# Optimization experiments

Hardware: AMD Instinct MI355X
Metric: run time of the kernel (lower is better)

## Reference

```python
import jax, jax.numpy as jnp
import numpy as np

TEMPERATURE = 0.07
EPS = 1e-12  # matches torch F.normalize default eps


def setup_inputs() -> dict:
    key = jax.random.key(0)
    k1, k2 = jax.random.split(key)
    features1 = jax.random.normal(k1, (16384, 512), dtype=jnp.float32)
    features2 = jax.random.normal(k2, (16384, 512), dtype=jnp.float32)
    return {"features1": features1, "features2": features2}


def _l2_normalize(x):
    # torch F.normalize: x / max(||x||, eps)
    norm = jnp.sqrt(jnp.sum(x * x, axis=1, keepdims=True))
    return x / jnp.maximum(norm, EPS)


def reference(features1, features2):
    f1 = _l2_normalize(features1)
    f2 = _l2_normalize(features2)
    # [N, N] similarity logits
    logits = jnp.einsum('nd,md->nm', f1, f2) / TEMPERATURE
    n = logits.shape[0]
    # cross-entropy with labels = arange(n): mean over rows of (logsumexp - diag logit)
    log_probs = jax.nn.log_softmax(logits, axis=1)
    diag = jnp.diagonal(log_probs)
    loss = -jnp.mean(diag)
    return loss
```

## Files before the change

kernel.cpp:

```cpp
#include <hip/hip_runtime.h>
#include <stdint.h>

#define NROWS 16384
#define KDIM  512
#define BM 128
#define BN 256
#define CT 2
#define NCHUNK 32
#define NPH 16
#define SLOT 24576
#define INV_T 14.285714285714286f
#define LOG2E 1.4426950408889634f
#define LN2   0.6931471805599453f

typedef __bf16 bf16x8 __attribute__((ext_vector_type(8)));
typedef float  f32x16 __attribute__((ext_vector_type(16)));
typedef unsigned short u16x8 __attribute__((ext_vector_type(8)));

__device__ __forceinline__ void gload_lds16(const void* gptr, void* lptr) {
    uint32_t loff = (uint32_t)(uintptr_t)lptr;
    loff = __builtin_amdgcn_readfirstlane(loff);
    __builtin_amdgcn_global_load_lds(
        (const uint32_t __attribute__((address_space(1)))*)(uintptr_t)gptr,
        (uint32_t __attribute__((address_space(3)))*)(uintptr_t)loff,
        16, 0, 0);
}


__global__ void k_norm(const float* __restrict__ X, char* __restrict__ Y, float scale) {
    const int row  = blockIdx.x * 4 + (threadIdx.x >> 6);
    const int lane = threadIdx.x & 63;
    const float* xr = X + (size_t)row * KDIM + lane * 8;
    float4 a = *(const float4*)xr;
    float4 b = *(const float4*)(xr + 4);
    float ss = a.x*a.x + a.y*a.y + a.z*a.z + a.w*a.w
             + b.x*b.x + b.y*b.y + b.z*b.z + b.w*b.w;
    #pragma unroll
    for (int off = 1; off < 64; off <<= 1) ss += __shfl_xor(ss, off);
    const float s = scale / fmaxf(sqrtf(ss), 1e-12f);
    __bf16 o[8];
    o[0] = (__bf16)(a.x * s); o[1] = (__bf16)(a.y * s);
    o[2] = (__bf16)(a.z * s); o[3] = (__bf16)(a.w * s);
    o[4] = (__bf16)(b.x * s); o[5] = (__bf16)(b.y * s);
    o[6] = (__bf16)(b.z * s); o[7] = (__bf16)(b.w * s);
    const int kh = lane >> 2, q = lane & 3;
    const size_t gr = ((size_t)(kh * 512 + (row >> 5)) * 2 + (q >> 1)) * 64
                    + ((q & 1) << 5) + (row & 31);
    *(u16x8*)(Y + gr * 16) = *(const u16x8*)o;
}

__global__ __launch_bounds__(256, 1) void k_gemm(const char* __restrict__ A,
                                                 const char* __restrict__ B,
                                                 float* __restrict__ S_part) {
    __shared__ __align__(16) char L[3 * SLOT];
    __shared__ float rowsum[2][BM];
    char* Lc = (char*)L;

    const int tid  = threadIdx.x;
    const int lane = tid & 63;
    const int w    = tid >> 6;
    const int wr   = w >> 1, wc = w & 1;
    const int bid  = blockIdx.x;
    const int xcd  = bid & 7;
    const int idx  = bid >> 3;
    const int st   = idx >> 5;
    const int wsub = idx & 31;
    const int sg   = xcd * 16 + st;
    const int bg   = sg & 15, cg = sg >> 4;
    const int brow  = (bg * 8 + (wsub >> 2)) * BM;
    const int chunk = cg * 4 + (wsub & 3);
    const int rbA0 = brow >> 5;

#define STGA(KH_, S_) do {                                                    \
        const char* g_ = A + ((size_t)((KH_) * 512 + rbA0) * 2048) + tid * 16;\
        char* l_ = Lc + (S_) * SLOT + tid * 16;                               \
        gload_lds16(g_,        l_);                                           \
        gload_lds16(g_ + 4096, l_ + 4096);                                    \
    } while (0)

#define STGB(KH_, S_) do {                                                    \
        const char* g_ = B + ((size_t)((KH_) * 512 + rbB0) * 2048) + tid * 16;\
        char* l_ = Lc + (S_) * SLOT + 8192 + tid * 16;                        \
        gload_lds16(g_,         l_);                                          \
        gload_lds16(g_ +  4096, l_ +  4096);                                  \
        gload_lds16(g_ +  8192, l_ +  8192);                                  \
        gload_lds16(g_ + 12288, l_ + 12288);                                  \
    } while (0)

#define RDS(HH_) do {                                                         \
        const char* sl_ = Lc + ((HH_) % 3) * SLOT;                            \
        _Pragma("unroll") for (int m_ = 0; m_ < 2; ++m_)                      \
        _Pragma("unroll") for (int ks_ = 0; ks_ < 2; ++ks_)                   \
            af[m_][ks_] = *(const bf16x8*)(sl_ + ((wr * 2 + m_) << 11)        \
                                           + (ks_ << 10) + (lane << 4));      \
        _Pragma("unroll") for (int n_ = 0; n_ < 4; ++n_)                      \
        _Pragma("unroll") for (int ks_ = 0; ks_ < 2; ++ks_)                   \
            bf[n_][ks_] = *(const bf16x8*)(sl_ + 8192                         \
                  + ((wc * 4 + n_) << 11) + (ks_ << 10) + (lane << 4));       \
    } while (0)

#define MM() do {                                                             \
        __builtin_amdgcn_s_setprio(1);                                        \
        _Pragma("unroll") for (int m_ = 0; m_ < 2; ++m_)                      \
        _Pragma("unroll") for (int n_ = 0; n_ < 4; ++n_)                      \
        _Pragma("unroll") for (int ks_ = 0; ks_ < 2; ++ks_)                   \
            acc[m_][n_] = __builtin_amdgcn_mfma_f32_32x32x16_bf16(            \
                af[m_][ks_], bf[n_][ks_], acc[m_][n_], 0, 0, 0);              \
        __builtin_amdgcn_s_setprio(0);                                        \
    } while (0)

    float rowacc = 0.f;
    #pragma unroll 1
    for (int ct = 0; ct < CT; ++ct) {
        const int rbB0 = chunk * 16 + ct * 8;
        f32x16 acc[2][4] = {};
        bf16x8 af[2][2], bf[4][2];

        STGA(0, 0); STGB(0, 0);
        STGA(1, 1); STGB(1, 1);
        asm volatile("s_waitcnt vmcnt(6)" ::: "memory");
        __builtin_amdgcn_s_barrier();

        #pragma unroll
        for (int h = 0; h < NPH; ++h) {
            RDS(h);
            if (h < NPH - 2) { STGA(h + 2, (h + 2) % 3); STGB(h + 2, (h + 2) % 3); }
            MM();
            if (h < NPH - 2)       asm volatile("s_waitcnt vmcnt(6)" ::: "memory");
            else if (h == NPH - 2) asm volatile("s_waitcnt vmcnt(0)" ::: "memory");
            __builtin_amdgcn_s_barrier();
        }

        #pragma unroll
        for (int m = 0; m < 2; ++m) {
            float rs[16];
            #pragma unroll
            for (int r = 0; r < 16; ++r)
                rs[r] = __builtin_amdgcn_exp2f(acc[m][0][r])
                      + __builtin_amdgcn_exp2f(acc[m][1][r])
                      + __builtin_amdgcn_exp2f(acc[m][2][r])
                      + __builtin_amdgcn_exp2f(acc[m][3][r]);
            #pragma unroll
            for (int off = 16; off >= 1; off >>= 1)
                #pragma unroll
                for (int r = 0; r < 16; ++r)
                    rs[r] += __shfl_xor(rs[r], off);
            if ((lane & 31) == 0) {
                const int rb = wr * 64 + m * 32 + (lane >> 5) * 4;
                #pragma unroll
                for (int r = 0; r < 16; ++r)
                    rowsum[wc][rb + (r & 3) + 8 * (r >> 2)] = rs[r];
            }
        }
        __syncthreads();
        if (tid < BM) rowacc += rowsum[0][tid] + rowsum[1][tid];
        __syncthreads();
    }
#undef STGA
#undef STGB
#undef RDS
#undef MM
    if (tid < BM) S_part[(size_t)chunk * NROWS + brow + tid] = rowacc;
}

__global__ void k_diag(const char* __restrict__ A, const char* __restrict__ B,
                       float* __restrict__ diag) {
    const int row  = blockIdx.x * 4 + (threadIdx.x >> 6);
    const int lane = threadIdx.x & 63;
    const int kh = lane >> 2, q = lane & 3;
    const size_t gr = ((size_t)(kh * 512 + (row >> 5)) * 2 + (q >> 1)) * 64
                    + ((q & 1) << 5) + (row & 31);
    const bf16x8 va = *(const bf16x8*)(A + gr * 16);
    const bf16x8 vb = *(const bf16x8*)(B + gr * 16);
    float d = 0.f;
    #pragma unroll
    for (int i = 0; i < 8; ++i) d += (float)va[i] * (float)vb[i];
    #pragma unroll
    for (int off2 = 1; off2 < 64; off2 <<= 1) d += __shfl_xor(d, off2);
    if (lane == 0) diag[row] = d;
}

__global__ void k_loss(const float* __restrict__ S_part, const float* __restrict__ diag,
                       float* __restrict__ partial) {
    const int g = blockIdx.x * 256 + threadIdx.x;
    float S = 0.f;
    #pragma unroll
    for (int c = 0; c < NCHUNK; ++c) S += S_part[(size_t)c * NROWS + g];
    float v = logf(S) - diag[g] * LN2;
    __shared__ float wsum[4];
    #pragma unroll
    for (int off = 1; off < 64; off <<= 1) v += __shfl_xor(v, off);
    if ((threadIdx.x & 63) == 0) wsum[threadIdx.x >> 6] = v;
    __syncthreads();
    if (threadIdx.x == 0) partial[blockIdx.x] = wsum[0] + wsum[1] + wsum[2] + wsum[3];
}

__global__ void k_final(const float* __restrict__ partial, float* __restrict__ out) {
    float v = partial[threadIdx.x];
    #pragma unroll
    for (int off = 1; off < 64; off <<= 1) v += __shfl_xor(v, off);
    if (threadIdx.x == 0) out[0] = v * (1.0f / (float)NROWS);
}

extern "C" void kernel_launch(void* const* d_in, const int* in_sizes, int n_in,
                              void* d_out, int out_size, void* d_ws, size_t ws_size,
                              hipStream_t stream) {
    const float* f1 = (const float*)d_in[0];
    const float* f2 = (const float*)d_in[1];
    float* out = (float*)d_out;

    char* ws = (char*)d_ws;
    char*  f1p   = ws;
    char*  f2p   = ws + (16u << 20);
    float* S_part = (float*)(ws + (32u << 20));
    float* diag   = (float*)(ws + (34u << 20));
    float* part   = (float*)(ws + (34u << 20) + (1u << 16));

    k_norm<<<dim3(NROWS / 4), dim3(256), 0, stream>>>(f1, f1p, INV_T * LOG2E);
    k_norm<<<dim3(NROWS / 4), dim3(256), 0, stream>>>(f2, f2p, 1.0f);
    k_gemm<<<dim3((NROWS / BM) * NCHUNK), dim3(256), 0, stream>>>(f1p, f2p, S_part);
    k_diag<<<dim3(NROWS / 4), dim3(256), 0, stream>>>(f1p, f2p, diag);
    k_loss<<<dim3(NROWS / 256), dim3(256), 0, stream>>>(S_part, diag, part);
    k_final<<<dim3(1), dim3(64), 0, stream>>>(part, out);
}
```

Before: 341.7 us.

## Restructure GEMM: register-resident A from global, half-K B staging in LDS

The logsumexp GEMM now uses 256-row blocks where each wave loads its A fragments straight from global memory into a rotating register pipeline. B is staged in LDS in two 64 KB half-K buffers that are double-buffered across four column sub-chunks, which cuts per-phase barriers and lets row sums accumulate in registers instead of going through shared memory. The diagonal kernel now computes the fp32 cosine directly from the raw inputs, so the bf16 diagonal no longer matches the bf16 GEMM logits. This trades fewer LDS round-trips and barriers for higher register pressure and uncached global A loads inside the MFMA loop.

```diff
diff --git a/kernel.cpp b/kernel.cpp
--- a/kernel.cpp
+++ b/kernel.cpp
@@ -3,15 +3,10 @@
 
 #define NROWS 16384
 #define KDIM  512
-#define BM 128
-#define BN 256
-#define CT 2
+#define BM 256
 #define NCHUNK 32
-#define NPH 16
-#define SLOT 24576
 #define INV_T 14.285714285714286f
 #define LOG2E 1.4426950408889634f
-#define LN2   0.6931471805599453f
 
 typedef __bf16 bf16x8 __attribute__((ext_vector_type(8)));
 typedef float  f32x16 __attribute__((ext_vector_type(16)));
@@ -52,84 +47,77 @@
 __global__ __launch_bounds__(256, 1) void k_gemm(const char* __restrict__ A,
                                                  const char* __restrict__ B,
                                                  float* __restrict__ S_part) {
-    __shared__ __align__(16) char L[3 * SLOT];
-    __shared__ float rowsum[2][BM];
+    __shared__ __align__(16) char L[2 * 65536];
     char* Lc = (char*)L;
 
     const int tid  = threadIdx.x;
     const int lane = tid & 63;
     const int w    = tid >> 6;
-    const int wr   = w >> 1, wc = w & 1;
     const int bid  = blockIdx.x;
     const int xcd  = bid & 7;
     const int idx  = bid >> 3;
     const int st   = idx >> 5;
     const int wsub = idx & 31;
-    const int sg   = xcd * 16 + st;
-    const int bg   = sg & 15, cg = sg >> 4;
+    const int sg   = xcd * 8 + st;
+    const int bg   = sg & 7, cg = sg >> 3;
     const int brow  = (bg * 8 + (wsub >> 2)) * BM;
     const int chunk = cg * 4 + (wsub & 3);
     const int rbA0 = brow >> 5;
 
-#define STGA(KH_, S_) do {                                                    \
-        const char* g_ = A + ((size_t)((KH_) * 512 + rbA0) * 2048) + tid * 16;\
-        char* l_ = Lc + (S_) * SLOT + tid * 16;                               \
-        gload_lds16(g_,        l_);                                           \
-        gload_lds16(g_ + 4096, l_ + 4096);                                    \
-    } while (0)
-
-#define STGB(KH_, S_) do {                                                    \
-        const char* g_ = B + ((size_t)((KH_) * 512 + rbB0) * 2048) + tid * 16;\
-        char* l_ = Lc + (S_) * SLOT + 8192 + tid * 16;                        \
-        gload_lds16(g_,         l_);                                          \
-        gload_lds16(g_ +  4096, l_ +  4096);                                  \
-        gload_lds16(g_ +  8192, l_ +  8192);                                  \
-        gload_lds16(g_ + 12288, l_ + 12288);                                  \
-    } while (0)
-
-#define RDS(HH_) do {                                                         \
-        const char* sl_ = Lc + ((HH_) % 3) * SLOT;                            \
+#define STGH(C_, KH0_, BUFOFF_) do {                                          \
+        const int rbB_ = chunk * 16 + (C_) * 4;                               \
+        _Pragma("unroll") for (int kk_ = 0; kk_ < 8; ++kk_) {                 \
+            const char* g_ = B + ((size_t)(((KH0_) + kk_) * 512 + rbB_) * 2048) + tid * 16; \
+            char* l_ = Lc + (BUFOFF_) + kk_ * 8192 + tid * 16;                \
+            gload_lds16(g_, l_);                                              \
+            gload_lds16(g_ + 4096, l_ + 4096);                                \
+        }                                                                     \
+    } while (0)
+
+#define LOADA(KH0_, T_, S_) do {                                              \
         _Pragma("unroll") for (int m_ = 0; m_ < 2; ++m_)                      \
-        _Pragma("unroll") for (int ks_ = 0; ks_ < 2; ++ks_)                   \
-            af[m_][ks_] = *(const bf16x8*)(sl_ + ((wr * 2 + m_) << 11)        \
-                                           + (ks_ << 10) + (lane << 4));      \
+            aF[S_][m_] = *(const bf16x8*)(A                                   \
+                + ((size_t)((((KH0_) + ((T_) >> 1)) * 512 + rbA0 + w * 2 + m_) * 2 \
+                            + ((T_) & 1)) << 10) + (lane << 4));              \
+    } while (0)
+
+#define READB(T_, BUFOFF_, S_) do {                                           \
         _Pragma("unroll") for (int n_ = 0; n_ < 4; ++n_)                      \
-        _Pragma("unroll") for (int ks_ = 0; ks_ < 2; ++ks_)                   \
-            bf[n_][ks_] = *(const bf16x8*)(sl_ + 8192                         \
-                  + ((wc * 4 + n_) << 11) + (ks_ << 10) + (lane << 4));       \
-    } while (0)
-
-#define MM() do {                                                             \
-        __builtin_amdgcn_s_setprio(1);                                        \
-        _Pragma("unroll") for (int m_ = 0; m_ < 2; ++m_)                      \
-        _Pragma("unroll") for (int n_ = 0; n_ < 4; ++n_)                      \
-        _Pragma("unroll") for (int ks_ = 0; ks_ < 2; ++ks_)                   \
-            acc[m_][n_] = __builtin_amdgcn_mfma_f32_32x32x16_bf16(            \
-                af[m_][ks_], bf[n_][ks_], acc[m_][n_], 0, 0, 0);              \
-        __builtin_amdgcn_s_setprio(0);                                        \
-    } while (0)
-
-    float rowacc = 0.f;
+            bF[S_][n_] = *(const bf16x8*)(Lc + (BUFOFF_)                      \
+                + (((T_) >> 1) * 8192) + (n_ * 2048)                          \
+                + (((T_) & 1) << 10) + (lane << 4));                          \
+    } while (0)
+
+#define HALF(KH0_, BUFOFF_, STG_STMT_) do {                                   \
+        LOADA(KH0_, 0, 0); LOADA(KH0_, 1, 1); LOADA(KH0_, 2, 2);              \
+        LOADA(KH0_, 3, 3); LOADA(KH0_, 4, 4); LOADA(KH0_, 5, 5);              \
+        STG_STMT_;                                                            \
+        READB(0, BUFOFF_, 0);                                                 \
+        _Pragma("unroll") for (int tt_ = 0; tt_ < 16; ++tt_) {                \
+            if (tt_ < 15) READB(tt_ + 1, BUFOFF_, (tt_ + 1) & 1);             \
+            if (tt_ < 10) LOADA(KH0_, tt_ + 6, (tt_ + 6) % 6);                \
+            _Pragma("unroll") for (int m_ = 0; m_ < 2; ++m_)                  \
+            _Pragma("unroll") for (int n_ = 0; n_ < 4; ++n_)                  \
+                acc[m_][n_] = __builtin_amdgcn_mfma_f32_32x32x16_bf16(        \
+                    aF[tt_ % 6][m_], bF[tt_ & 1][n_], acc[m_][n_], 0, 0, 0);  \
+        }                                                                     \
+    } while (0)
+
+    bf16x8 aF[6][2], bF[2][4];
+    float rowacc[2][16] = {};
+
+    STGH(0, 0, 0);
+    asm volatile("s_waitcnt vmcnt(0)" ::: "memory");
+    __builtin_amdgcn_s_barrier();
+
     #pragma unroll 1
-    for (int ct = 0; ct < CT; ++ct) {
-        const int rbB0 = chunk * 16 + ct * 8;
+    for (int c = 0; c < 4; ++c) {
         f32x16 acc[2][4] = {};
-        bf16x8 af[2][2], bf[4][2];
-
-        STGA(0, 0); STGB(0, 0);
-        STGA(1, 1); STGB(1, 1);
-        asm volatile("s_waitcnt vmcnt(6)" ::: "memory");
+        HALF(0, 0, STGH(c, 8, 65536));
+        asm volatile("s_waitcnt vmcnt(0)" ::: "memory");
         __builtin_amdgcn_s_barrier();
-
-        #pragma unroll
-        for (int h = 0; h < NPH; ++h) {
-            RDS(h);
-            if (h < NPH - 2) { STGA(h + 2, (h + 2) % 3); STGB(h + 2, (h + 2) % 3); }
-            MM();
-            if (h < NPH - 2)       asm volatile("s_waitcnt vmcnt(6)" ::: "memory");
-            else if (h == NPH - 2) asm volatile("s_waitcnt vmcnt(0)" ::: "memory");
-            __builtin_amdgcn_s_barrier();
-        }
+        if (c < 3) { HALF(8, 65536, STGH(c + 1, 0, 0)); }
+        else       { HALF(8, 65536, ((void)0)); }
 
         #pragma unroll
         for (int m = 0; m < 2; ++m) {
@@ -145,39 +133,50 @@
                 #pragma unroll
                 for (int r = 0; r < 16; ++r)
                     rs[r] += __shfl_xor(rs[r], off);
-            if ((lane & 31) == 0) {
-                const int rb = wr * 64 + m * 32 + (lane >> 5) * 4;
-                #pragma unroll
-                for (int r = 0; r < 16; ++r)
-                    rowsum[wc][rb + (r & 3) + 8 * (r >> 2)] = rs[r];
-            }
+            #pragma unroll
+            for (int r = 0; r < 16; ++r) rowacc[m][r] += rs[r];
         }
-        __syncthreads();
-        if (tid < BM) rowacc += rowsum[0][tid] + rowsum[1][tid];
-        __syncthreads();
+        asm volatile("s_waitcnt vmcnt(0)" ::: "memory");
+        __builtin_amdgcn_s_barrier();
     }
-#undef STGA
-#undef STGB
-#undef RDS
-#undef MM
-    if (tid < BM) S_part[(size_t)chunk * NROWS + brow + tid] = rowacc;
-}
-
-__global__ void k_diag(const char* __restrict__ A, const char* __restrict__ B,
+#undef STGH
+#undef LOADA
+#undef READB
+#undef HALF
+
+    if ((lane & 31) == 0) {
+        const int hi = lane >> 5;
+        #pragma unroll
+        for (int m = 0; m < 2; ++m)
+            #pragma unroll
+            for (int r = 0; r < 16; ++r)
+                S_part[(size_t)chunk * NROWS + brow + w * 64 + m * 32
+                       + hi * 4 + (r & 3) + 8 * (r >> 2)] = rowacc[m][r];
+    }
+}
+
+__global__ void k_diag(const float* __restrict__ X1, const float* __restrict__ X2,
                        float* __restrict__ diag) {
     const int row  = blockIdx.x * 4 + (threadIdx.x >> 6);
     const int lane = threadIdx.x & 63;
-    const int kh = lane >> 2, q = lane & 3;
-    const size_t gr = ((size_t)(kh * 512 + (row >> 5)) * 2 + (q >> 1)) * 64
-                    + ((q & 1) << 5) + (row & 31);
-    const bf16x8 va = *(const bf16x8*)(A + gr * 16);
-    const bf16x8 vb = *(const bf16x8*)(B + gr * 16);
-    float d = 0.f;
-    #pragma unroll
-    for (int i = 0; i < 8; ++i) d += (float)va[i] * (float)vb[i];
-    #pragma unroll
-    for (int off2 = 1; off2 < 64; off2 <<= 1) d += __shfl_xor(d, off2);
-    if (lane == 0) diag[row] = d;
+    const float* x1 = X1 + (size_t)row * KDIM + lane * 8;
+    const float* x2 = X2 + (size_t)row * KDIM + lane * 8;
+    float4 a0 = *(const float4*)x1, a1 = *(const float4*)(x1 + 4);
+    float4 b0 = *(const float4*)x2, b1 = *(const float4*)(x2 + 4);
+    float s1 = a0.x*a0.x + a0.y*a0.y + a0.z*a0.z + a0.w*a0.w
+             + a1.x*a1.x + a1.y*a1.y + a1.z*a1.z + a1.w*a1.w;
+    float s2 = b0.x*b0.x + b0.y*b0.y + b0.z*b0.z + b0.w*b0.w
+             + b1.x*b1.x + b1.y*b1.y + b1.z*b1.z + b1.w*b1.w;
+    float dd = a0.x*b0.x + a0.y*b0.y + a0.z*b0.z + a0.w*b0.w
+             + a1.x*b1.x + a1.y*b1.y + a1.z*b1.z + a1.w*b1.w;
+    #pragma unroll
+    for (int off = 1; off < 64; off <<= 1) {
+        s1 += __shfl_xor(s1, off);
+        s2 += __shfl_xor(s2, off);
+        dd += __shfl_xor(dd, off);
+    }
+    if (lane == 0)
+        diag[row] = dd / (fmaxf(sqrtf(s1), 1e-12f) * fmaxf(sqrtf(s2), 1e-12f)) * INV_T;
 }
 
 __global__ void k_loss(const float* __restrict__ S_part, const float* __restrict__ diag,
@@ -186,7 +185,7 @@
     float S = 0.f;
     #pragma unroll
     for (int c = 0; c < NCHUNK; ++c) S += S_part[(size_t)c * NROWS + g];
-    float v = logf(S) - diag[g] * LN2;
+    float v = logf(S) - diag[g];
     __shared__ float wsum[4];
     #pragma unroll
     for (int off = 1; off < 64; off <<= 1) v += __shfl_xor(v, off);
@@ -219,7 +218,7 @@
     k_norm<<<dim3(NROWS / 4), dim3(256), 0, stream>>>(f1, f1p, INV_T * LOG2E);
     k_norm<<<dim3(NROWS / 4), dim3(256), 0, stream>>>(f2, f2p, 1.0f);
     k_gemm<<<dim3((NROWS / BM) * NCHUNK), dim3(256), 0, stream>>>(f1p, f2p, S_part);
-    k_diag<<<dim3(NROWS / 4), dim3(256), 0, stream>>>(f1p, f2p, diag);
+    k_diag<<<dim3(NROWS / 4), dim3(256), 0, stream>>>(f1, f2, diag);
     k_loss<<<dim3(NROWS / 256), dim3(256), 0, stream>>>(S_part, diag, part);
     k_final<<<dim3(1), dim3(64), 0, stream>>>(part, out);
 }
```

Result: slower. 725.1 us (+112.2%).
